# Performance work log

Measured on AMD Instinct MI355X. Metric: run time of the kernel, lower is better.

The kernel has to match this reference:

```python
import jax, jax.numpy as jnp
import numpy as np

HIDDEN = 1024
HEADS = 16
HEAD_DIM = HIDDEN // HEADS


def setup_inputs() -> dict:
    key = jax.random.key(0)
    ks = jax.random.split(key, 5)
    x = jax.random.normal(ks[0], (4, 2048, HIDDEN), dtype=jnp.float32)
    s = 1.0 / np.sqrt(HIDDEN)
    W_qkv = jax.random.normal(ks[1], (HIDDEN, 3 * HIDDEN), dtype=jnp.float32) * s
    b_qkv = jax.random.normal(ks[2], (3 * HIDDEN,), dtype=jnp.float32) * s
    W_out = jax.random.normal(ks[3], (HIDDEN, HIDDEN), dtype=jnp.float32) * s
    b_out = jax.random.normal(ks[4], (HIDDEN,), dtype=jnp.float32) * s
    return {"x": x, "W_qkv": W_qkv, "b_qkv": b_qkv, "W_out": W_out, "b_out": b_out}


def reference(x, W_qkv, b_qkv, W_out, b_out):
    B, S, _ = x.shape
    qkv = x @ W_qkv + b_qkv                       # [B,S,3H]
    qkv = qkv.reshape(B, S, 3, HEADS, HEAD_DIM)
    q, k, v = jnp.moveaxis(qkv, 2, 0)             # each [B,S,nh,hd]
    scale = 1.0 / np.sqrt(HEAD_DIM)
    scores = jnp.einsum('bqhd,bkhd->bhqk', q, k) * scale
    probs = jax.nn.softmax(scores, axis=-1)       # dropout p=0 (eval): identity
    attn = jnp.einsum('bhqk,bkhd->bqhd', probs, v)
    attn = attn.reshape(B, S, HIDDEN)
    return attn @ W_out + b_out
```

## Files before the change

kernel.cpp:

```cpp
#include <hip/hip_runtime.h>

#define SEQ    2048
#define BATCH  4
#define HID    1024
#define NH     16
#define MTOT   (BATCH * SEQ)

typedef __attribute__((ext_vector_type(8)))  short          short8;
typedef __attribute__((ext_vector_type(4)))  float          f32x4;
typedef __attribute__((ext_vector_type(16))) float          f32x16;
typedef __attribute__((ext_vector_type(8)))  unsigned short ushort8v;
typedef __attribute__((ext_vector_type(4)))  unsigned int   uint4v;

#define QSCL 0.125f

__device__ __forceinline__ float bf2f(unsigned short u) {
    return __uint_as_float(((unsigned int)u) << 16);
}
__device__ __forceinline__ unsigned short f2bf(float f) {
    unsigned int u = __float_as_uint(f);
    u += 0x7fffu + ((u >> 16) & 1u);
    return (unsigned short)(u >> 16);
}
__device__ __forceinline__ unsigned int pk2bf(float lo, float hi) {
    unsigned int ul = __float_as_uint(lo) + 0x8000u;
    unsigned int uh = __float_as_uint(hi) + 0x8000u;
    return __builtin_amdgcn_perm(uh, ul, 0x07060302u);
}

__device__ __forceinline__ void gl_lds16(const void* g, void* l) {
    __builtin_amdgcn_global_load_lds(
        (__attribute__((address_space(1))) void*)g,
        (__attribute__((address_space(3))) void*)l, 16, 0, 0);
}

__device__ __forceinline__ int swz64(int row, int col) {
    return row * 64 + ((((col >> 3) ^ (row & 7))) << 3) + (col & 7);
}

__device__ __forceinline__ int gidx64(int row, int kq) {
    return (row * 8 + ((kq + (row & 7)) & 7)) * 8;
}

__global__ __launch_bounds__(256)
void cvt_x(const float* __restrict__ x, unsigned short* __restrict__ xb)
{
    const size_t i = ((size_t)blockIdx.x * 256 + threadIdx.x) * 4;
    const float4 f = *(const float4*)(x + i);
    uint2 u;
    u.x = pk2bf(f.x, f.y);
    u.y = pk2bf(f.z, f.w);
    *(uint2*)(xb + i) = u;
}

__global__ __launch_bounds__(256)
void transpose_cvt(const float* __restrict__ W, unsigned short* __restrict__ Wt,
                   int K, int N)
{
    __shared__ unsigned short T[32][33];
    const int n0 = blockIdx.x * 32, k0 = blockIdx.y * 32;
    const int tr = threadIdx.x >> 3, tc = (threadIdx.x & 7) * 4;
    const float4 f = *(const float4*)(W + (size_t)(k0 + tr) * N + n0 + tc);
    T[tr][tc + 0] = f2bf(f.x);
    T[tr][tc + 1] = f2bf(f.y);
    T[tr][tc + 2] = f2bf(f.z);
    T[tr][tc + 3] = f2bf(f.w);
    __syncthreads();
    ushort4 u;
    u.x = T[tc + 0][tr]; u.y = T[tc + 1][tr];
    u.z = T[tc + 2][tr]; u.w = T[tc + 3][tr];
    *(ushort4*)(Wt + (size_t)(n0 + tr) * K + k0 + tc) = u;
}

template<bool OUTF32, bool VSPLIT, bool BIASROW>
__global__ __launch_bounds__(256)
void gemm_mfma(const unsigned short* __restrict__ A,
               const unsigned short* __restrict__ Bt,
               const float* __restrict__ bias, void* __restrict__ Cptr,
               int lda, int ldc, int K)
{
    __shared__ unsigned short As[128 * 64];
    __shared__ unsigned short Bs[128 * 64];

    const int tid = threadIdx.x;
    const int wave = tid >> 6, lane = tid & 63;
    const int quad = lane >> 4, lm = lane & 15;
    const int wm = wave & 1, wn = wave >> 1;

    const int nwg = gridDim.x * gridDim.y;
    const int bid = blockIdx.y * gridDim.x + blockIdx.x;
    const int swz = (bid & 7) * (nwg >> 3) + (bid >> 3);
    const int m0 = (swz / gridDim.x) * 128;
    const int n0 = (swz % gridDim.x) * 128;

    const unsigned short* aSrc[4];
    const unsigned short* bSrc[4];
    unsigned short* aDst[4];
    unsigned short* bDst[4];
    #pragma unroll
    for (int j = 0; j < 4; ++j) {
        const int g = (wave * 4 + j) * 64 + lane;
        const int row = g >> 3;
        const int kq = ((g & 7) - (row & 7)) & 7;
        aSrc[j] = A  + (size_t)(m0 + row) * lda + kq * 8;
        bSrc[j] = Bt + (size_t)(n0 + row) * K   + kq * 8;
        aDst[j] = &As[g * 8];
        bDst[j] = &Bs[g * 8];
    }

    f32x4 acc[4][4];
    #pragma unroll
    for (int i = 0; i < 4; ++i)
        #pragma unroll
        for (int j = 0; j < 4; ++j)
            acc[i][j] = (f32x4){0.f, 0.f, 0.f, 0.f};

    int aOff[2][4], bOff[2][4];
    #pragma unroll
    for (int h = 0; h < 2; ++h)
        #pragma unroll
        for (int i = 0; i < 4; ++i) {
            aOff[h][i] = gidx64(wm * 64 + i * 16 + lm, h * 4 + quad);
            bOff[h][i] = gidx64(wn * 64 + i * 16 + lm, h * 4 + quad);
        }

    for (int k0 = 0; k0 < K; k0 += 64) {
        __syncthreads();
        #pragma unroll
        for (int j = 0; j < 4; ++j) gl_lds16(aSrc[j] + k0, aDst[j]);
        #pragma unroll
        for (int j = 0; j < 4; ++j) gl_lds16(bSrc[j] + k0, bDst[j]);
        __syncthreads();

        #pragma unroll
        for (int h = 0; h < 2; ++h) {
            short8 af[4], bf[4];
            #pragma unroll
            for (int i = 0; i < 4; ++i) af[i] = *(const short8*)&As[aOff[h][i]];
            #pragma unroll
            for (int j = 0; j < 4; ++j) bf[j] = *(const short8*)&Bs[bOff[h][j]];
            #pragma unroll
            for (int i = 0; i < 4; ++i)
                #pragma unroll
                for (int j = 0; j < 4; ++j)
                    acc[i][j] = __builtin_amdgcn_mfma_f32_16x16x32_bf16(
                        af[i], bf[j], acc[i][j], 0, 0, 0);
        }
    }

    float bj[4];
    float br[4][4];
    if constexpr (BIASROW) {
        #pragma unroll
        for (int i = 0; i < 4; ++i) {
            const float4 t =
                *(const float4*)(bias + m0 + wm * 64 + i * 16 + quad * 4);
            br[i][0] = t.x; br[i][1] = t.y; br[i][2] = t.z; br[i][3] = t.w;
        }
    } else {
        #pragma unroll
        for (int j = 0; j < 4; ++j) bj[j] = bias[n0 + wn * 64 + j * 16 + lm];
    }

    #pragma unroll
    for (int i = 0; i < 4; ++i) {
        #pragma unroll
        for (int j = 0; j < 4; ++j) {
            const int col = n0 + wn * 64 + j * 16 + lm;
            #pragma unroll
            for (int rr = 0; rr < 4; ++rr) {
                const int row = m0 + wm * 64 + i * 16 + quad * 4 + rr;
                float v = acc[i][j][rr] + (BIASROW ? br[i][rr] : bj[j]);
                if constexpr (VSPLIT) {
                    if (col < 1024) v *= QSCL;
                    ((unsigned short*)Cptr)[(size_t)row * ldc + col] = f2bf(v);
                } else if constexpr (OUTF32) {
                    ((float*)Cptr)[(size_t)row * ldc + col] = v;
                } else {
                    ((unsigned short*)Cptr)[(size_t)row * ldc + col] = f2bf(v);
                }
            }
        }
    }
}

__global__ __launch_bounds__(256, 2)
void attn_mfma(unsigned short* __restrict__ qk,
               const unsigned short* __restrict__ Vt)
{
    const int bid = blockIdx.x;
    const int qt = bid >> 6;
    const int g  = bid & 63;
    const int hh = g & 15;
    const int b  = g >> 4;
    const size_t row0 = (size_t)b * SEQ;
    const int tid = threadIdx.x;
    const int wave = tid >> 6, lane = tid & 63;
    const int l5 = lane >> 5, lm = lane & 31;

    __shared__ unsigned short Ks[2][64 * 64];
    __shared__ unsigned short Vs[2][64 * 64];

    const int qbase = qt * 256 + wave * 64;

    short8 qf[2][4];
    #pragma unroll
    for (int qg = 0; qg < 2; ++qg)
        #pragma unroll
        for (int ks = 0; ks < 4; ++ks)
            qf[qg][ks] = *(const short8*)(
                qk + (row0 + qbase + qg * 32 + lm) * 2048 + hh * 64 + ks * 16 + l5 * 8);

    f32x16 oacc[2][2];
    #pragma unroll
    for (int dg = 0; dg < 2; ++dg)
        #pragma unroll
        for (int qg = 0; qg < 2; ++qg)
            #pragma unroll
            for (int e = 0; e < 16; ++e) oacc[dg][qg][e] = 0.f;
    float lrun[2] = {0.f, 0.f};

    const unsigned short* kSrc[2];
    const unsigned short* vSrc[2];
    int dOff[2];
    #pragma unroll
    for (int jj = 0; jj < 2; ++jj) {
        const int gg = (wave * 2 + jj) * 64 + lane;
        const int row = gg >> 3, slot = gg & 7;
        const int colg = slot ^ (row & 7);
        kSrc[jj] = qk + 1024 + hh * 64 + (row0 + row) * 2048 + colg * 8;
        vSrc[jj] = Vt + (size_t)(hh * 64 + row) * (size_t)MTOT
                      + (size_t)b * SEQ + colg * 8;
        dOff[jj] = gg * 8;
    }

    #pragma unroll
    for (int jj = 0; jj < 2; ++jj) {
        gl_lds16(kSrc[jj], &Ks[0][dOff[jj]]);
        gl_lds16(vSrc[jj], &Vs[0][dOff[jj]]);
    }
    __syncthreads();

    int cur = 0;
    for (int kt = 0; kt < SEQ; kt += 64) {
        if (kt + 64 < SEQ) {
            const size_t ko = (size_t)(kt + 64) * 2048;
            const int vo = kt + 64;
            #pragma unroll
            for (int jj = 0; jj < 2; ++jj) {
                gl_lds16(kSrc[jj] + ko, &Ks[cur ^ 1][dOff[jj]]);
                gl_lds16(vSrc[jj] + vo, &Vs[cur ^ 1][dOff[jj]]);
            }
        }
        const unsigned short* ksc = Ks[cur];
        const unsigned short* vsc = Vs[cur];

        #pragma unroll
        for (int kg = 0; kg < 2; ++kg) {
            short8 aK[4];
            #pragma unroll
            for (int ks = 0; ks < 4; ++ks)
                aK[ks] = *(const short8*)&ksc[swz64(kg * 32 + lm, ks * 16 + l5 * 8)];

            f32x16 s[2];
            #pragma unroll
            for (int qg = 0; qg < 2; ++qg) {
                #pragma unroll
                for (int e = 0; e < 16; ++e) s[qg][e] = 0.f;
                __builtin_amdgcn_s_setprio(1);
                #pragma unroll
                for (int ks = 0; ks < 4; ++ks)
                    s[qg] = __builtin_amdgcn_mfma_f32_32x32x16_bf16(
                        aK[ks], qf[qg][ks], s[qg], 0, 0, 0);
                __builtin_amdgcn_s_setprio(0);
                float ls = 0.f;
                #pragma unroll
                for (int rg = 0; rg < 4; ++rg) {
                    const float p0 = __expf(s[qg][rg * 4 + 0]);
                    const float p1 = __expf(s[qg][rg * 4 + 1]);
                    const float p2 = __expf(s[qg][rg * 4 + 2]);
                    const float p3 = __expf(s[qg][rg * 4 + 3]);
                    s[qg][rg * 4 + 0] = p0; s[qg][rg * 4 + 1] = p1;
                    s[qg][rg * 4 + 2] = p2; s[qg][rg * 4 + 3] = p3;
                    ls += (p0 + p1) + (p2 + p3);
                }
                lrun[qg] += ls;
            }

            #pragma unroll
            for (int step = 0; step < 2; ++step) {
                const int ks = kg * 2 + step;
                const short8 aV0 =
                    *(const short8*)&vsc[swz64(lm,      ks * 16 + l5 * 8)];
                const short8 aV1 =
                    *(const short8*)&vsc[swz64(32 + lm, ks * 16 + l5 * 8)];
                #pragma unroll
                for (int qg = 0; qg < 2; ++qg) {
                    const int b0 = step * 8;
                    const unsigned int u  = pk2bf(s[qg][b0 + 0], s[qg][b0 + 1]);
                    const unsigned int vv = pk2bf(s[qg][b0 + 2], s[qg][b0 + 3]);
                    const unsigned int u2 = pk2bf(s[qg][b0 + 4], s[qg][b0 + 5]);
                    const unsigned int v2 = pk2bf(s[qg][b0 + 6], s[qg][b0 + 7]);
                    const auto rA =
                        __builtin_amdgcn_permlane32_swap(u,  u2, false, false);
                    const auto rB =
                        __builtin_amdgcn_permlane32_swap(vv, v2, false, false);
                    uint4v wv;
                    wv.x = rA[0]; wv.y = rB[0]; wv.z = rA[1]; wv.w = rB[1];
                    const short8 bP = __builtin_bit_cast(short8, wv);
                    __builtin_amdgcn_s_setprio(1);
                    oacc[0][qg] = __builtin_amdgcn_mfma_f32_32x32x16_bf16(
                        aV0, bP, oacc[0][qg], 0, 0, 0);
                    oacc[1][qg] = __builtin_amdgcn_mfma_f32_32x32x16_bf16(
                        aV1, bP, oacc[1][qg], 0, 0, 0);
                    __builtin_amdgcn_s_setprio(0);
                }
            }
        }
        __syncthreads();
        cur ^= 1;
    }

    float linv[2];
    #pragma unroll
    for (int qg = 0; qg < 2; ++qg) {
        const float lt = lrun[qg] + __shfl_xor(lrun[qg], 32);
        linv[qg] = 1.f / lt;
    }

    #pragma unroll
    for (int dg = 0; dg < 2; ++dg)
        #pragma unroll
        for (int qg = 0; qg < 2; ++qg) {
            unsigned short* orow =
                qk + (row0 + qbase + qg * 32 + lm) * 2048 + hh * 64;
            #pragma unroll
            for (int rg = 0; rg < 4; ++rg) {
                const int d0 = dg * 32 + rg * 8 + l5 * 4;
                ushort4 st;
                st.x = f2bf(oacc[dg][qg][rg * 4 + 0] * linv[qg]);
                st.y = f2bf(oacc[dg][qg][rg * 4 + 1] * linv[qg]);
                st.z = f2bf(oacc[dg][qg][rg * 4 + 2] * linv[qg]);
                st.w = f2bf(oacc[dg][qg][rg * 4 + 3] * linv[qg]);
                *(ushort4*)(orow + d0) = st;
            }
        }
}

__global__ __launch_bounds__(256)
void qproj(const float* __restrict__ A, const float* __restrict__ W,
           const float* __restrict__ bias, unsigned short* __restrict__ outus)
{
    __shared__ float As[64][17];
    __shared__ float Bs[16][64];
    const int tid = threadIdx.x;
    const int tx = tid & 15, ty = tid >> 4;
    const int m0 = blockIdx.y * 64, n0 = blockIdx.x * 64;
    const int ar = tid >> 2, ac = (tid & 3) * 4;
    const int br = tid >> 4, bc = (tid & 15) * 4;
    float acc[4][4] = {{0.f}};
    for (int k0 = 0; k0 < HID; k0 += 16) {
        const float4 av = *(const float4*)(A + (size_t)(m0 + ar) * HID + k0 + ac);
        As[ar][ac + 0] = av.x; As[ar][ac + 1] = av.y;
        As[ar][ac + 2] = av.z; As[ar][ac + 3] = av.w;
        *(float4*)&Bs[br][bc] =
            *(const float4*)(W + (size_t)(k0 + br) * 3072 + n0 + bc);
        __syncthreads();
        #pragma unroll
        for (int kk = 0; kk < 16; ++kk) {
            float a[4];
            #pragma unroll
            for (int i = 0; i < 4; ++i) a[i] = As[ty * 4 + i][kk];
            const float4 b4 = *(const float4*)&Bs[kk][tx * 4];
            const float bv[4] = {b4.x, b4.y, b4.z, b4.w};
            #pragma unroll
            for (int i = 0; i < 4; ++i)
                #pragma unroll
                for (int j = 0; j < 4; ++j)
                    acc[i][j] = fmaf(a[i], bv[j], acc[i][j]);
        }
        __syncthreads();
    }
    float bb[4];
    #pragma unroll
    for (int j = 0; j < 4; ++j) bb[j] = bias[n0 + tx * 4 + j];
    #pragma unroll
    for (int i = 0; i < 4; ++i) {
        ushort4 st;
        st.x = f2bf(acc[i][0] + bb[0]); st.y = f2bf(acc[i][1] + bb[1]);
        st.z = f2bf(acc[i][2] + bb[2]); st.w = f2bf(acc[i][3] + bb[3]);
        *(ushort4*)(outus + (size_t)(m0 + ty * 4 + i) * 2048 + 1024 + n0 + tx * 4) = st;
    }
}

__global__ __launch_bounds__(256)
void kv_inplace(const float* __restrict__ W, const float* __restrict__ bias,
                unsigned short* __restrict__ xu)
{
    const float* xf = (const float*)xu;
    __shared__ unsigned short Asb[16][1032];
    __shared__ float Bs[16][68];
    const int tid = threadIdx.x;
    const int m0 = blockIdx.x * 16;
    const int tx = tid & 15, ty = tid >> 4;
    #pragma unroll 4
    for (int i = 0; i < 16; ++i) {
        const float4 v = *(const float4*)(xf + (size_t)(m0 + i) * HID + tid * 4);
        ushort4 s;
        s.x = f2bf(v.x); s.y = f2bf(v.y); s.z = f2bf(v.z); s.w = f2bf(v.w);
        *(ushort4*)&Asb[i][tid * 4] = s;
    }
    __syncthreads();
    for (int n0 = 0; n0 < 2048; n0 += 64) {
        float acc[4] = {0.f, 0.f, 0.f, 0.f};
        for (int k0 = 0; k0 < HID; k0 += 16) {
            *(float4*)&Bs[ty][tx * 4] =
                *(const float4*)(W + (size_t)(k0 + ty) * 3072 + 1024 + n0 + tx * 4);
            __syncthreads();
            #pragma unroll
            for (int kk = 0; kk < 16; ++kk) {
                const float a = bf2f(Asb[ty][k0 + kk]);
                const float4 b4 = *(const float4*)&Bs[kk][tx * 4];
                acc[0] = fmaf(a, b4.x, acc[0]); acc[1] = fmaf(a, b4.y, acc[1]);
                acc[2] = fmaf(a, b4.z, acc[2]); acc[3] = fmaf(a, b4.w, acc[3]);
            }
            __syncthreads();
        }
        const int n = n0 + tx * 4;
        ushort4 s;
        s.x = f2bf(acc[0] + bias[1024 + n + 0]);
        s.y = f2bf(acc[1] + bias[1024 + n + 1]);
        s.z = f2bf(acc[2] + bias[1024 + n + 2]);
        s.w = f2bf(acc[3] + bias[1024 + n + 3]);
        *(ushort4*)(xu + (size_t)(m0 + ty) * 2048 + n) = s;
    }
}

__global__ __launch_bounds__(256)
void attn_fwd(const unsigned short* __restrict__ xu,
              unsigned short* __restrict__ outus)
{
    const int qt = blockIdx.x, h = blockIdx.y, b = blockIdx.z;
    const int s0 = qt * 16;
    const size_t row0 = (size_t)b * SEQ;
    const int tid = threadIdx.x;
    const int qi = tid >> 4, tj = tid & 15;
    __shared__ float Ksh[64][68];
    __shared__ float Vsh[64][68];
    __shared__ float Psh[16][68];
    float qreg[64];
    {
        const uint4* qp =
            (const uint4*)(outus + (row0 + s0 + qi) * 2048 + 1024 + h * 64);
        #pragma unroll
        for (int i = 0; i < 8; ++i) {
            uint4 u = qp[i];
            const unsigned int w[4] = {u.x, u.y, u.z, u.w};
            #pragma unroll
            for (int j = 0; j < 4; ++j) {
                qreg[i * 8 + j * 2 + 0] = __uint_as_float(w[j] << 16) * 0.125f;
                qreg[i * 8 + j * 2 + 1] = __uint_as_float(w[j] & 0xffff0000u) * 0.125f;
            }
        }
    }
    float mrun = -1e30f, lrunv = 0.f;
    float oacc[4] = {0.f, 0.f, 0.f, 0.f};
    const int lr = tid >> 3, lc = (tid & 7) * 8;
    for (int kt = 0; kt < SEQ; kt += 64) {
        __syncthreads();
        #pragma unroll
        for (int half = 0; half < 2; ++half) {
            const int r = lr + half * 32;
            const size_t rowoff = (row0 + kt + r) * 2048 + h * 64 + lc;
            uint4 ku = *(const uint4*)(xu + rowoff);
            uint4 vu = *(const uint4*)(xu + rowoff + 1024);
            float4 f0, f1;
            f0.x = __uint_as_float(ku.x << 16); f0.y = __uint_as_float(ku.x & 0xffff0000u);
            f0.z = __uint_as_float(ku.y << 16); f0.w = __uint_as_float(ku.y & 0xffff0000u);
            f1.x = __uint_as_float(ku.z << 16); f1.y = __uint_as_float(ku.z & 0xffff0000u);
            f1.z = __uint_as_float(ku.w << 16); f1.w = __uint_as_float(ku.w & 0xffff0000u);
            *(float4*)&Ksh[r][lc]     = f0;
            *(float4*)&Ksh[r][lc + 4] = f1;
            f0.x = __uint_as_float(vu.x << 16); f0.y = __uint_as_float(vu.x & 0xffff0000u);
            f0.z = __uint_as_float(vu.y << 16); f0.w = __uint_as_float(vu.y & 0xffff0000u);
            f1.x = __uint_as_float(vu.z << 16); f1.y = __uint_as_float(vu.z & 0xffff0000u);
            f1.z = __uint_as_float(vu.w << 16); f1.w = __uint_as_float(vu.w & 0xffff0000u);
            *(float4*)&Vsh[r][lc]     = f0;
            *(float4*)&Vsh[r][lc + 4] = f1;
        }
        __syncthreads();
        float sc[4];
        #pragma unroll
        for (int u = 0; u < 4; ++u) {
            const int kk = tj + 16 * u;
            float s = 0.f;
            #pragma unroll
            for (int d = 0; d < 64; ++d) s = fmaf(qreg[d], Ksh[kk][d], s);
            sc[u] = s;
        }
        float tmax = fmaxf(fmaxf(sc[0], sc[1]), fmaxf(sc[2], sc[3]));
        #pragma unroll
        for (int off = 8; off >= 1; off >>= 1)
            tmax = fmaxf(tmax, __shfl_xor(tmax, off, 16));
        const float mnew = fmaxf(mrun, tmax);
        const float alpha = __expf(mrun - mnew);
        float psum = 0.f;
        #pragma unroll
        for (int u = 0; u < 4; ++u) {
            const float p = __expf(sc[u] - mnew);
            Psh[qi][tj + 16 * u] = p;
            psum += p;
        }
        #pragma unroll
        for (int off = 8; off >= 1; off >>= 1)
            psum += __shfl_xor(psum, off, 16);
        lrunv = lrunv * alpha + psum;
        mrun = mnew;
        oacc[0] *= alpha; oacc[1] *= alpha; oacc[2] *= alpha; oacc[3] *= alpha;
        __syncthreads();
        #pragma unroll 8
        for (int kk = 0; kk < 64; ++kk) {
            const float p = Psh[qi][kk];
            const float4 v4 = *(const float4*)&Vsh[kk][tj * 4];
            oacc[0] = fmaf(p, v4.x, oacc[0]); oacc[1] = fmaf(p, v4.y, oacc[1]);
            oacc[2] = fmaf(p, v4.z, oacc[2]); oacc[3] = fmaf(p, v4.w, oacc[3]);
        }
    }
    const float inv = 1.f / lrunv;
    ushort4 st;
    st.x = f2bf(oacc[0] * inv); st.y = f2bf(oacc[1] * inv);
    st.z = f2bf(oacc[2] * inv); st.w = f2bf(oacc[3] * inv);
    *(ushort4*)(outus + (row0 + s0 + qi) * 2048 + h * 64 + tj * 4) = st;
}

__global__ __launch_bounds__(256)
void out_final(const float* __restrict__ W, const float* __restrict__ bias,
               unsigned short* __restrict__ outus)
{
    float* outf = (float*)outus;
    __shared__ unsigned short Asb[16][1032];
    __shared__ float Bs[16][68];
    const int tid = threadIdx.x;
    const int m0 = blockIdx.x * 16;
    const int tx = tid & 15, ty = tid >> 4;
    #pragma unroll 4
    for (int i = 0; i < 16; ++i)
        *(ushort4*)&Asb[i][tid * 4] =
            *(const ushort4*)(outus + (size_t)(m0 + i) * 2048 + tid * 4);
    __syncthreads();
    for (int n0 = 0; n0 < 1024; n0 += 64) {
        float acc[4] = {0.f, 0.f, 0.f, 0.f};
        for (int k0 = 0; k0 < HID; k0 += 16) {
            *(float4*)&Bs[ty][tx * 4] =
                *(const float4*)(W + (size_t)(k0 + ty) * HID + n0 + tx * 4);
            __syncthreads();
            #pragma unroll
            for (int kk = 0; kk < 16; ++kk) {
                const float a = bf2f(Asb[ty][k0 + kk]);
                const float4 b4 = *(const float4*)&Bs[kk][tx * 4];
                acc[0] = fmaf(a, b4.x, acc[0]); acc[1] = fmaf(a, b4.y, acc[1]);
                acc[2] = fmaf(a, b4.z, acc[2]); acc[3] = fmaf(a, b4.w, acc[3]);
            }
            __syncthreads();
        }
        const int n = n0 + tx * 4;
        float4 st;
        st.x = acc[0] + bias[n + 0]; st.y = acc[1] + bias[n + 1];
        st.z = acc[2] + bias[n + 2]; st.w = acc[3] + bias[n + 3];
        *(float4*)(outf + (size_t)(m0 + ty) * HID + n) = st;
    }
}

extern "C" void kernel_launch(void* const* d_in, const int* in_sizes, int n_in,
                              void* d_out, int out_size, void* d_ws, size_t ws_size,
                              hipStream_t stream) {
    const float* x     = (const float*)d_in[0];
    const float* W_qkv = (const float*)d_in[1];
    const float* b_qkv = (const float*)d_in[2];
    const float* W_out = (const float*)d_in[3];
    const float* b_out = (const float*)d_in[4];

    dim3 blk(256);

    if (ws_size >= (size_t)56 * 1024 * 1024) {
        unsigned short* qkbuf  = (unsigned short*)d_ws;
        unsigned short* vtbuf  = qkbuf + (size_t)MTOT * 2048;
        unsigned short* wqkv_t = vtbuf + (size_t)1024 * MTOT;
        unsigned short* wout_t = wqkv_t + (size_t)3072 * 1024;
        unsigned short* xb     = (unsigned short*)d_out;

        cvt_x<<<dim3(MTOT * HID / 1024), blk, 0, stream>>>(x, xb);
        transpose_cvt<<<dim3(3072 / 32, 1024 / 32), blk, 0, stream>>>(
            W_qkv, wqkv_t, 1024, 3072);
        transpose_cvt<<<dim3(1024 / 32, 1024 / 32), blk, 0, stream>>>(
            W_out, wout_t, 1024, 1024);
        gemm_mfma<false, true, false><<<dim3(2048 / 128, MTOT / 128), blk, 0, stream>>>(
            xb, wqkv_t, b_qkv, (void*)qkbuf, 1024, 2048, 1024);
        gemm_mfma<false, false, true><<<dim3(MTOT / 128, 1024 / 128), blk, 0, stream>>>(
            wqkv_t + (size_t)2048 * 1024, xb, b_qkv + 2048, (void*)vtbuf,
            1024, MTOT, 1024);
        attn_mfma<<<dim3(512), blk, 0, stream>>>(qkbuf, vtbuf);
        gemm_mfma<true, false, false><<<dim3(1024 / 128, MTOT / 128), blk, 0, stream>>>(
            qkbuf, wout_t, b_out, d_out, 2048, 1024, 1024);
    } else {
        unsigned short* outus = (unsigned short*)d_out;
        unsigned short* xu    = (unsigned short*)d_in[0];
        qproj<<<dim3(HID / 64, MTOT / 64), blk, 0, stream>>>(x, W_qkv, b_qkv, outus);
        kv_inplace<<<dim3(MTOT / 16), blk, 0, stream>>>(W_qkv, b_qkv, xu);
        attn_fwd<<<dim3(SEQ / 16, NH, BATCH), blk, 0, stream>>>(xu, outus);
        out_final<<<dim3(MTOT / 16), blk, 0, stream>>>(W_out, b_out, outus);
    }
}
```

Measured before the change: 276.3 us.

## Add 256x256-tile 8-wave pipelined GEMM for QK projection

Replaces the 128x128 QK projection GEMM with a dedicated kernel that uses 512 threads and 256x256 output tiles. It double-buffers LDS halves via direct global-to-LDS loads interleaved across four compute phases, with explicit barriers, vmcnt waits and setprio around the MFMA blocks. It also swizzles the block order for L2 locality. This raises data reuse per tile and overlaps loads with MFMA, at the cost of higher register pressure (128 accumulator floats per lane), a 128 KB LDS footprint, one block per CU, and only 256 blocks to fill the device.

Measured after the change: 275.1 us. About the same (-0.5%).

```diff
diff --git a/kernel.cpp b/kernel.cpp
--- a/kernel.cpp
+++ b/kernel.cpp
@@ -70,6 +70,143 @@
     u.x = T[tc + 0][tr]; u.y = T[tc + 1][tr];
     u.z = T[tc + 2][tr]; u.w = T[tc + 3][tr];
     *(ushort4*)(Wt + (size_t)(n0 + tr) * K + k0 + tc) = u;
+}
+
+__global__ __launch_bounds__(512, 1)
+void gemm_qk8(const unsigned short* __restrict__ A,
+              const unsigned short* __restrict__ Bt,
+              const float* __restrict__ bias,
+              unsigned short* __restrict__ C)
+{
+    __shared__ unsigned short Asl[2][2][128 * 64];
+    __shared__ unsigned short Bsl[2][2][128 * 64];
+
+    const int tid  = threadIdx.x;
+    const int wave = tid >> 6, lane = tid & 63;
+    const int quad = lane >> 4, lm = lane & 15;
+    const int wm = wave >> 2, wn = wave & 3;
+
+    const int bid = blockIdx.x;
+    const int swz = (bid & 7) * 32 + (bid >> 3);
+    const int m0 = (swz >> 3) * 256;
+    const int n0 = (swz & 7) * 256;
+
+    int rowg[2], kqg[2], dofs[2];
+#pragma unroll
+    for (int j = 0; j < 2; ++j) {
+        const int g = (j * 8 + wave) * 64 + lane;
+        const int r = g >> 3;
+        rowg[j] = r;
+        kqg[j]  = (((g & 7) - (r & 7)) & 7) * 8;
+        dofs[j] = g * 8;
+    }
+
+#define STG_A(BUFD, H, K0)                                                   \
+    _Pragma("unroll")                                                        \
+    for (int j = 0; j < 2; ++j)                                              \
+        gl_lds16(A + (size_t)(m0 + (H) * 128 + rowg[j]) * 1024 + kqg[j] + (K0), \
+                 &Asl[BUFD][H][dofs[j]]);
+#define STG_B(BUFD, H, K0)                                                   \
+    _Pragma("unroll")                                                        \
+    for (int j = 0; j < 2; ++j)                                              \
+        gl_lds16(Bt + (size_t)(n0 + (H) * 128 + rowg[j]) * 1024 + kqg[j] + (K0), \
+                 &Bsl[BUFD][H][dofs[j]]);
+
+    f32x4 acc[8][4];
+#pragma unroll
+    for (int m = 0; m < 8; ++m)
+#pragma unroll
+        for (int n = 0; n < 4; ++n)
+            acc[m][n] = (f32x4){0.f, 0.f, 0.f, 0.f};
+
+    int aOff[4][2], bOff[2][2];
+#pragma unroll
+    for (int i = 0; i < 4; ++i)
+#pragma unroll
+        for (int kh = 0; kh < 2; ++kh)
+            aOff[i][kh] = gidx64(i * 32 + wm * 16 + lm, kh * 4 + quad);
+#pragma unroll
+    for (int j = 0; j < 2; ++j)
+#pragma unroll
+        for (int kh = 0; kh < 2; ++kh)
+            bOff[j][kh] = gidx64(j * 64 + wn * 16 + lm, kh * 4 + quad);
+
+#define PHASE(AH, BH, STAGE_STMT, VMJ)                                       \
+    {                                                                        \
+        short8 aF[4][2], bF[2][2];                                           \
+        _Pragma("unroll")                                                    \
+        for (int i = 0; i < 4; ++i)                                          \
+            _Pragma("unroll")                                                \
+            for (int kh = 0; kh < 2; ++kh)                                   \
+                aF[i][kh] = *(const short8*)&Asl[cur][AH][aOff[i][kh]];      \
+        _Pragma("unroll")                                                    \
+        for (int j = 0; j < 2; ++j)                                          \
+            _Pragma("unroll")                                                \
+            for (int kh = 0; kh < 2; ++kh)                                   \
+                bF[j][kh] = *(const short8*)&Bsl[cur][BH][bOff[j][kh]];      \
+        STAGE_STMT                                                           \
+        asm volatile("s_barrier" ::: "memory");                              \
+        asm volatile("s_waitcnt lgkmcnt(0)" ::: "memory");                   \
+        __builtin_amdgcn_s_setprio(1);                                       \
+        _Pragma("unroll")                                                    \
+        for (int kh = 0; kh < 2; ++kh)                                       \
+            _Pragma("unroll")                                                \
+            for (int i = 0; i < 4; ++i)                                      \
+                _Pragma("unroll")                                            \
+                for (int j = 0; j < 2; ++j)                                  \
+                    acc[(AH) * 4 + i][(BH) * 2 + j] =                        \
+                        __builtin_amdgcn_mfma_f32_16x16x32_bf16(             \
+                            aF[i][kh], bF[j][kh],                            \
+                            acc[(AH) * 4 + i][(BH) * 2 + j], 0, 0, 0);       \
+        __builtin_amdgcn_s_setprio(0);                                       \
+        VMJ                                                                  \
+        asm volatile("s_barrier" ::: "memory");                              \
+    }
+
+#define VM_CNT                                                               \
+    if (more) { asm volatile("s_waitcnt vmcnt(4)" ::: "memory"); }           \
+    else      { asm volatile("s_waitcnt vmcnt(0)" ::: "memory"); }
+
+    STG_A(0, 0, 0)
+    STG_B(0, 0, 0)
+    STG_B(0, 1, 0)
+    STG_A(0, 1, 0)
+    asm volatile("s_waitcnt vmcnt(4)" ::: "memory");
+    asm volatile("s_barrier" ::: "memory");
+
+    for (int t = 0; t < 16; ++t) {
+        const int cur = t & 1, nxt = cur ^ 1;
+        const bool more = (t < 15);
+        const int k1 = (t + 1) * 64;
+
+        PHASE(0, 0, if (more) { STG_A(nxt, 0, k1) }, VM_CNT)
+        PHASE(0, 1, if (more) { STG_B(nxt, 0, k1) }, VM_CNT)
+        PHASE(1, 0, if (more) { STG_B(nxt, 1, k1) }, VM_CNT)
+        PHASE(1, 1, if (more) { STG_A(nxt, 1, k1) }, VM_CNT)
+    }
+#undef PHASE
+#undef VM_CNT
+#undef STG_A
+#undef STG_B
+
+    float bj[4];
+#pragma unroll
+    for (int n = 0; n < 4; ++n) bj[n] = bias[n0 + wn * 16 + n * 64 + lm];
+
+#pragma unroll
+    for (int m = 0; m < 8; ++m) {
+#pragma unroll
+        for (int n = 0; n < 4; ++n) {
+            const int col = n0 + wn * 16 + n * 64 + lm;
+#pragma unroll
+            for (int rr = 0; rr < 4; ++rr) {
+                const int row = m0 + wm * 16 + m * 32 + quad * 4 + rr;
+                float v = acc[m][n][rr] + bj[n];
+                if (col < 1024) v *= QSCL;
+                C[(size_t)row * 2048 + col] = f2bf(v);
+            }
+        }
+    }
 }
 
 template<bool OUTF32, bool VSPLIT, bool BIASROW>
@@ -594,8 +731,8 @@
             W_qkv, wqkv_t, 1024, 3072);
         transpose_cvt<<<dim3(1024 / 32, 1024 / 32), blk, 0, stream>>>(
             W_out, wout_t, 1024, 1024);
-        gemm_mfma<false, true, false><<<dim3(2048 / 128, MTOT / 128), blk, 0, stream>>>(
-            xb, wqkv_t, b_qkv, (void*)qkbuf, 1024, 2048, 1024);
+        gemm_qk8<<<dim3(256), dim3(512), 0, stream>>>(
+            xb, wqkv_t, b_qkv, qkbuf);
         gemm_mfma<false, false, true><<<dim3(MTOT / 128, 1024 / 128), blk, 0, stream>>>(
             wqkv_t + (size_t)2048 * 1024, xb, b_qkv + 2048, (void*)vtbuf,
             1024, MTOT, 1024);
```
